# Kernel optimization log

Hardware: AMD Instinct MI355X
Metric: run time of the kernel (lower is better)

## Reference

```python
import jax, jax.numpy as jnp
import numpy as np

M = N = 768
Q = 32
P_ROW = P_COL = 4
NB_ITER = 3


def cheb_basis(L, order):
    # Chebyshev polynomials T_k(L), stacked -> (order+1, n, n)
    n = L.shape[0]
    Ts = [jnp.eye(n, dtype=L.dtype)]
    if order > 0:
        Ts.append(L)
    for _ in range(2, order + 1):
        Ts.append(2.0 * (L @ Ts[-1]) - Ts[-2])
    return jnp.stack(Ts)


def setup_inputs() -> dict:
    key = jax.random.key(0)
    ks = jax.random.split(key, 24)
    f32 = jnp.float32
    # scaled symmetric Laplacians with small spectral radius (keeps Cheb recursion stable)
    Ar = jax.random.normal(ks[0], (M, M), dtype=f32)
    L_row = (Ar + Ar.T) / (2.0 * jnp.sqrt(jnp.float32(M)))
    Ac = jax.random.normal(ks[1], (N, N), dtype=f32)
    L_col = (Ac + Ac.T) / (2.0 * jnp.sqrt(jnp.float32(N)))
    x = jax.random.normal(ks[2], (M, N), dtype=f32)
    theta = 0.05 * jax.random.normal(ks[3], (P_ROW + 1, P_COL + 1, Q), dtype=f32)
    bias = jnp.zeros((Q,), dtype=f32)
    s = 1.0 / np.sqrt(Q)
    def w(k):
        return s * jax.random.normal(k, (Q, Q), dtype=f32)
    inp = {
        'x': x, 'L_row': L_row, 'L_col': L_col, 'theta': theta, 'bias': bias,
        'W_f': w(ks[4]), 'U_f': w(ks[5]), 'b_f': jnp.zeros((Q,), f32),
        'W_i': w(ks[6]), 'U_i': w(ks[7]), 'b_i': jnp.zeros((Q,), f32),
        'W_o': w(ks[8]), 'U_o': w(ks[9]), 'b_o': jnp.zeros((Q,), f32),
        'W_c': w(ks[10]), 'U_c': w(ks[11]), 'b_c': jnp.zeros((Q,), f32),
        'W_out': s * jax.random.normal(ks[12], (Q, 1), dtype=f32),
        'b_out': jnp.zeros((1, 1), f32),
        'nb_iterations_rnn': NB_ITER,
    }
    return inp


def reference(x, L_row, L_col, theta, bias,
              W_f, U_f, b_f, W_i, U_i, b_i, W_o, U_o, b_o, W_c, U_c, b_c,
              W_out, b_out, nb_iterations_rnn):
    pr = theta.shape[0] - 1
    pc = theta.shape[1] - 1
    q = theta.shape[2]
    m, n = x.shape
    Tr = cheb_basis(L_row, pr)  # (pr+1, M, M)
    Tc = cheb_basis(L_col, pc)  # (pc+1, N, N)

    def conv(xx):
        xr = jnp.einsum('imp,pn->imn', Tr, xx)            # (pr+1, M, N)
        bf = jnp.einsum('imn,jnk->ijmk', xr, Tc)           # (pr+1, pc+1, M, N)
        return jnp.einsum('ijmn,ijo->omn', bf, theta) + bias[:, None, None]

    def step(carry, _):
        xx, h, c = carry
        xc = conv(xx).transpose(1, 2, 0).reshape(-1, q)    # (M*N, q)
        f = jax.nn.sigmoid(xc @ W_f + h @ U_f + b_f)
        i = jax.nn.sigmoid(xc @ W_i + h @ U_i + b_i)
        o = jax.nn.sigmoid(xc @ W_o + h @ U_o + b_o)
        cu = jax.nn.sigmoid(xc @ W_c + h @ U_c + b_c)      # note: sigmoid, as in source
        c = f * c + i * cu
        h = o * jax.nn.sigmoid(c)                           # note: sigmoid(c), as in source
        dx = jnp.tanh(c @ W_out + b_out).reshape(m, n)
        return (xx + dx, h, c), None

    h0 = jnp.zeros((m * n, q), dtype=x.dtype)
    c0 = jnp.zeros((m * n, q), dtype=x.dtype)
    (x_out, _, _), _ = jax.lax.scan(step, (x, h0, c0), None, length=int(nb_iterations_rnn))
    return x_out
```

## Files before the change

### kernel.cpp

```cpp
#include <hip/hip_runtime.h>
#include <hip/hip_bf16.h>
#include <stdint.h>


#define DIM 768
#define MXK 589824
#define STK 2949120

typedef _Float16 f16x8 __attribute__((ext_vector_type(8)));
typedef float f32x4 __attribute__((ext_vector_type(4)));
typedef unsigned short ushort_t;
typedef _Float16 f16_t;

__device__ __forceinline__ float sigm(float v) {
    float e = __expf(-v);
    return __builtin_amdgcn_rcpf(1.0f + e);
}
__device__ __forceinline__ void split2h(float f, f16_t& h1, f16_t& h2) {
    h1 = (f16_t)f;
    h2 = (f16_t)(f - (float)h1);
}

__device__ __forceinline__ void gl_lds16(const f16_t* g, f16_t* l) {
    auto gp = reinterpret_cast<const __attribute__((address_space(1))) uint32_t*>(
        reinterpret_cast<uintptr_t>(g));
    auto lp = reinterpret_cast<__attribute__((address_space(3))) uint32_t*>(
        reinterpret_cast<uintptr_t>(l));
    __builtin_amdgcn_global_load_lds(gp, lp, 16, 0, 0);
}

__global__ __launch_bounds__(256) void init_split(
    const float* __restrict__ Lrow, const float* __restrict__ Lcol,
    f16_t* __restrict__ S0, f16_t* __restrict__ S1)
{
    int idx = blockIdx.x * 256 + threadIdx.x;
    int p = idx / DIM, m = idx % DIM;
    f16_t eye = (p == m) ? (f16_t)1.0f : (f16_t)0.0f;
    S0[idx] = eye; S1[idx] = (f16_t)0.0f;
    S0[STK + idx] = eye; S1[STK + idx] = (f16_t)0.0f;
    f16_t h1, h2;
    split2h(Lrow[idx], h1, h2);
    S0[MXK + idx] = h1; S1[MXK + idx] = h2;
    split2h(Lcol[idx], h1, h2);
    S0[STK + MXK + idx] = h1; S1[STK + MXK + idx] = h2;
}

__global__ __launch_bounds__(256) void prep_gate(
    const float* __restrict__ Wf, const float* __restrict__ Wi,
    const float* __restrict__ Wo, const float* __restrict__ Wc,
    const float* __restrict__ Uf, const float* __restrict__ Ui,
    const float* __restrict__ Uo, const float* __restrict__ Uc,
    const float* __restrict__ theta, const float* __restrict__ biasv,
    f16_t* __restrict__ Wstack, f16_t* __restrict__ thstack)
{
    int idx = blockIdx.x * 256 + threadIdx.x;
    if (idx < 8192) {
        int R = idx >> 6, k = idx & 63;
        int g = (R >> 4) & 3, o = (R >> 6) * 16 + (R & 15);
        const float* Wg[4] = {Wf, Wi, Wo, Wc};
        const float* Ug[4] = {Uf, Ui, Uo, Uc};
        float v = (k < 32) ? Wg[g][k * 32 + o] : Ug[g][(k - 32) * 32 + o];
        Wstack[idx] = (f16_t)v;
    } else if (idx < 9216) {
        int t = idx - 8192;
        int o = t >> 5, k = t & 31;
        float v = (k < 25) ? theta[k * 32 + o]
                           : (k == 25 ? biasv[o] : 0.0f);
        thstack[o * 32 + k] = (f16_t)v;
    }
}

__global__ __launch_bounds__(256) void transpose_cvt2x(
    const float* __restrict__ in, f16_t* __restrict__ o1,
    f16_t* __restrict__ o2, f16_t* __restrict__ xr0,
    f16_t* __restrict__ Cbf)
{
    __shared__ float t[32][33];
    int x = threadIdx.x & 31, y = threadIdx.x >> 5;
    int bx = blockIdx.x * 32, by = blockIdx.y * 32;
#pragma unroll
    for (int r = 0; r < 4; ++r) {
        int p = by + y + 8 * r, q = bx + x;
        size_t oi = (size_t)p * DIM + q;
        float v = in[oi];
        t[y + 8 * r][x] = v;
        f16_t hv = (f16_t)v;
        xr0[oi] = hv;
        Cbf[(size_t)p * 3840 + q] = hv;
    }
    __syncthreads();
#pragma unroll
    for (int r = 0; r < 4; ++r) {
        float v = t[x][y + 8 * r];
        f16_t h1, h2;
        split2h(v, h1, h2);
        size_t o = (size_t)(bx + y + 8 * r) * DIM + by + x;
        o1[o] = h1; o2[o] = h2;
    }
}

__global__ __launch_bounds__(256, 4) void gemm_bt_h2(
    const f16_t* __restrict__ A1,
    const f16_t* __restrict__ B1, const f16_t* __restrict__ B2,
    const f16_t* __restrict__ P1, const f16_t* __restrict__ P2,
    f16_t* __restrict__ D1, f16_t* __restrict__ D2, f16_t* __restrict__ D3,
    int K, int ldc, int mode, int nbx, int halfStride, int coloff)
{
    __shared__ __align__(16) f16_t sA[2][128 * 32];
    __shared__ __align__(16) f16_t sB[2][2 * 96 * 32];

    const int tid = threadIdx.x;
    const bool dual = (B2 != nullptr);

    int bx, by;
    size_t hoff = 0;
    int aoff = 0, boff = 0, poff = 0, doff = 0;
    if (mode == 3) {
        int g = blockIdx.x;
        int sup = g >> 8;
        int rows0 = sup * 8;
        int H = 30 - rows0; if (H > 8) H = 8;
        int local = g - rows0 * nbx;
        by = rows0 + local % H;
        bx = local / H;
    } else if (mode == 4) {
        int g = blockIdx.x;
        int t34 = g / 96, r = g % 96;
        int stack = r / 48, rr = r % 48;
        by = rr >> 3; bx = rr & 7;
        hoff = (size_t)stack * halfStride;
        if (t34 == 0) { aoff = MXK; boff = 2 * MXK; poff = MXK; doff = 3 * MXK; }
        else          { aoff = 2 * MXK; boff = 2 * MXK; poff = 0; doff = 4 * MXK; }
    } else {
        bx = blockIdx.x % nbx;
        by = blockIdx.x / nbx;
        if (mode == 2 && by >= 6) { by -= 6; hoff = (size_t)halfStride; }
    }
    const int m0 = by * 128, n0 = bx * 96;

    const f16_t* Asrc1 = A1 + hoff + aoff;
    const f16_t* Bsrc1 = B1 + hoff + boff;
    const f16_t* Bsrc2 = dual ? B2 + hoff + boff : nullptr;
    const f16_t* Pq1 = P1 ? P1 + hoff + poff : nullptr;
    const f16_t* Pq2 = P2 ? P2 + hoff + poff : nullptr;
    f16_t* Dq1 = D1 + hoff + doff;
    f16_t* Dq2 = D2 ? D2 + hoff + doff : nullptr;

    const int lane = tid & 63, w4 = tid >> 6;
    const int wm = (w4 & 1) * 64, wn = (w4 >> 1) * 48;
    const int lm = lane & 15, quad = lane >> 4;
    const int psw = (quad ^ ((lm >> 1) & 3)) * 8;

    const f16_t* gApt[2]; int aslot[2];
#pragma unroll
    for (int cc = 0; cc < 2; ++cc) {
        int s = cc * 256 + w4 * 64 + lane;
        int row = s >> 2, pos = s & 3;
        int chunk = pos ^ ((row >> 1) & 3);
        gApt[cc] = Asrc1 + (size_t)(m0 + row) * K + chunk * 8;
        aslot[cc] = s * 8;
    }
    const f16_t* gBpt[3]; int bslot[3]; bool bact[3];
#pragma unroll
    for (int cc = 0; cc < 3; ++cc) {
        int slot = cc * 256 + w4 * 64 + lane;
        bact[cc] = dual || (slot < 384);
        int lev = slot >= 384 ? 1 : 0;
        int s = slot - lev * 384;
        int row = s >> 2, pos = s & 3;
        int chunk = pos ^ ((row >> 1) & 3);
        const f16_t* bs = (lev && dual) ? Bsrc2 : Bsrc1;
        gBpt[cc] = bs + (size_t)(n0 + row) * K + chunk * 8;
        bslot[cc] = lev * 3072 + s * 8;
    }

    f32x4 acc[4][3] = {};

#pragma unroll
    for (int cc = 0; cc < 2; ++cc) gl_lds16(gApt[cc], &sA[0][aslot[cc]]);
#pragma unroll
    for (int cc = 0; cc < 3; ++cc)
        if (bact[cc]) gl_lds16(gBpt[cc], &sB[0][bslot[cc]]);
    __syncthreads();

    int ib = 0;
    for (int kb = 0; kb < K; kb += 32, ib ^= 1) {
        if (kb + 32 < K) {
            int nb = ib ^ 1;
#pragma unroll
            for (int cc = 0; cc < 2; ++cc)
                gl_lds16(gApt[cc] + kb + 32, &sA[nb][aslot[cc]]);
#pragma unroll
            for (int cc = 0; cc < 3; ++cc)
                if (bact[cc]) gl_lds16(gBpt[cc] + kb + 32, &sB[nb][bslot[cc]]);
        }

        f16x8 bfr[2][3];
#pragma unroll
        for (int fn = 0; fn < 3; ++fn)
            bfr[0][fn] = *(const f16x8*)&sB[ib][(wn + fn * 16 + lm) * 32 + psw];
        if (dual) {
#pragma unroll
            for (int fn = 0; fn < 3; ++fn)
                bfr[1][fn] = *(const f16x8*)&sB[ib][3072 +
                                                (wn + fn * 16 + lm) * 32 + psw];
        }
#pragma unroll
        for (int fm = 0; fm < 4; ++fm) {
            f16x8 a1v = *(const f16x8*)&sA[ib][(wm + fm * 16 + lm) * 32 + psw];
#pragma unroll
            for (int fn = 0; fn < 3; ++fn) {
                acc[fm][fn] = __builtin_amdgcn_mfma_f32_16x16x32_f16(
                    a1v, bfr[0][fn], acc[fm][fn], 0, 0, 0);
                if (dual)
                    acc[fm][fn] = __builtin_amdgcn_mfma_f32_16x16x32_f16(
                        a1v, bfr[1][fn], acc[fm][fn], 0, 0, 0);
            }
        }
        __syncthreads();
    }

#pragma unroll
    for (int fm = 0; fm < 4; ++fm)
#pragma unroll
        for (int fn = 0; fn < 3; ++fn) {
            int col = n0 + wn + fn * 16 + lm;
#pragma unroll
            for (int r = 0; r < 4; ++r) {
                int row = m0 + wm + fm * 16 + quad * 4 + r;
                float val = acc[fm][fn][r];
                if (mode == 3) {
                    Dq1[(size_t)row * ldc + coloff + col] = (f16_t)val;
                } else if (mode == 1) {
                    Dq1[(size_t)row * ldc + col] = (f16_t)val;
                    if (D3) D3[(size_t)row * 3840 + col] = (f16_t)val;
                } else {
                    size_t o = (size_t)row * ldc + col;
                    val = 2.0f * val - ((float)Pq1[o] + (float)Pq2[o]);
                    f16_t h1, h2;
                    split2h(val, h1, h2);
                    Dq1[o] = h1; Dq2[o] = h2;
                }
            }
        }
}

__global__ __launch_bounds__(256, 3) void gate_theta_mfma(
    const f16_t* __restrict__ Cbf, const f16_t* __restrict__ thstack,
    const f16_t* __restrict__ Wstack,
    const float* __restrict__ bfv, const float* __restrict__ biv,
    const float* __restrict__ bov, const float* __restrict__ bcv,
    const float* __restrict__ Wout, const float* __restrict__ bout,
    f16_t* __restrict__ h, f16_t* __restrict__ c, float* __restrict__ x,
    int first, int last)
{
    __shared__ __align__(16) ushort_t sC[2][26 * 128];
    __shared__ __align__(16) ushort_t sB[2][128 * 40];
    __shared__ float red[256];

    const int tid = threadIdx.x;
    const int lane = tid & 63, w4 = tid >> 6;
    const int wm = (w4 & 1) * 64, wn = (w4 >> 1) * 64;
    const int lm = lane & 15, quad = lane >> 4;
    const int m = blockIdx.x;
    const int o0 = (wm >> 2) + quad * 4;
    const int pw = w4 * 32;

    if (tid < 32) {
        uint4 ones;
        ones.x = ones.y = ones.z = ones.w = 0x3C003C00u;
        *(uint4*)&sC[tid >> 4][25 * 128 + (tid & 15) * 8] = ones;
    }

    auto stage = [&](int n0, int buf) {
#pragma unroll
        for (int cc = 0; cc < 2; ++cc) {
            int s = cc * 256 + tid;
            if (s < 400) {
                int ij = s >> 4, f = s & 15;
                int i5 = (ij * 205) >> 10;
                int j5 = ij - i5 * 5;
                size_t ga = (size_t)(i5 * DIM + m) * 3840 + j5 * DIM + n0 + f * 8;
                gl_lds16(&Cbf[ga], (f16_t*)&sC[buf][ij * 128 + f * 8]);
            }
        }
    };

    f16x8 bth[2];
#pragma unroll
    for (int fn = 0; fn < 2; ++fn)
        bth[fn] = *(const f16x8*)&thstack[(fn * 16 + lm) * 32 + quad * 8];
    f16x8 af[4][2];
#pragma unroll
    for (int fm = 0; fm < 4; ++fm)
#pragma unroll
        for (int kc = 0; kc < 2; ++kc)
            af[fm][kc] = *(const f16x8*)&Wstack[(wm + fm * 16 + lm) * 64 +
                                                kc * 32 + quad * 8];
    const float4 bgf = *(const float4*)&bfv[o0];
    const float4 bgi = *(const float4*)&biv[o0];
    const float4 bgo = *(const float4*)&bov[o0];
    const float4 bgc = *(const float4*)&bcv[o0];
    const float4 wo4 = *(const float4*)&Wout[o0];
    float bf4[4] = {bgf.x, bgf.y, bgf.z, bgf.w};
    float bi4[4] = {bgi.x, bgi.y, bgi.z, bgi.w};
    float bo4[4] = {bgo.x, bgo.y, bgo.z, bgo.w};
    float bc4[4] = {bgc.x, bgc.y, bgc.z, bgc.w};
    float wo[4] = {wo4.x, wo4.y, wo4.z, wo4.w};
    const float bout0 = bout[0];

    stage(0, 0);
    f16x8 hfr[4];
    f16_t cold[4][4];
    if (!first) {
#pragma unroll
        for (int fn = 0; fn < 4; ++fn) {
            size_t p = (size_t)(m * DIM + wn + fn * 16 + lm);
            hfr[fn] = *(const f16x8*)&h[p * 32 + quad * 8];
            *(uint2*)cold[fn] = *(const uint2*)&c[p * 32 + o0];
        }
    } else {
#pragma unroll
        for (int fn = 0; fn < 4; ++fn) {
#pragma unroll
            for (int j = 0; j < 8; ++j) hfr[fn][j] = (f16_t)0.0f;
#pragma unroll
            for (int r = 0; r < 4; ++r) cold[fn][r] = (f16_t)0.0f;
        }
    }
    __syncthreads();

    int tb = 0;
    for (int t = 0; t < 6; ++t, tb ^= 1) {
        const int n0 = t * 128;
        const int pbase = m * DIM + n0;

        {
            const f16_t* sCf = (const f16_t*)sC[tb];
            f32x4 tacc[2][2] = {};
            f16x8 a0, a1;
#pragma unroll
            for (int j = 0; j < 8; ++j) {
                int k = quad * 8 + j;
                int ij = k > 25 ? 25 : k;
                a0[j] = sCf[ij * 128 + pw + lm];
                a1[j] = sCf[ij * 128 + pw + 16 + lm];
            }
#pragma unroll
            for (int fn = 0; fn < 2; ++fn) {
                tacc[0][fn] = __builtin_amdgcn_mfma_f32_16x16x32_f16(
                    a0, bth[fn], tacc[0][fn], 0, 0, 0);
                tacc[1][fn] = __builtin_amdgcn_mfma_f32_16x16x32_f16(
                    a1, bth[fn], tacc[1][fn], 0, 0, 0);
            }
#pragma unroll
            for (int fm2 = 0; fm2 < 2; ++fm2)
#pragma unroll
                for (int fn = 0; fn < 2; ++fn)
#pragma unroll
                    for (int r = 0; r < 4; ++r) {
                        f16_t hv = (f16_t)tacc[fm2][fn][r];
                        sB[tb][(pw + fm2 * 16 + quad * 4 + r) * 40 +
                               fn * 16 + lm] = __builtin_bit_cast(ushort_t, hv);
                    }
        }
        __syncthreads();

        if (t < 5) stage(n0 + 128, tb ^ 1);
        f16x8 hfrn[4];
        f16_t coldn[4][4];
        if (t < 5 && !first) {
#pragma unroll
            for (int fn = 0; fn < 4; ++fn) {
                size_t p = (size_t)(pbase + 128 + wn + fn * 16 + lm);
                hfrn[fn] = *(const f16x8*)&h[p * 32 + quad * 8];
                *(uint2*)coldn[fn] = *(const uint2*)&c[p * 32 + o0];
            }
        } else {
#pragma unroll
            for (int fn = 0; fn < 4; ++fn) {
#pragma unroll
                for (int j = 0; j < 8; ++j) hfrn[fn][j] = (f16_t)0.0f;
#pragma unroll
                for (int r = 0; r < 4; ++r) coldn[fn][r] = (f16_t)0.0f;
            }
        }

#pragma unroll
        for (int fn = 0; fn < 4; ++fn) {
            f16x8 bxc = *(const f16x8*)&sB[tb][(wn + fn * 16 + lm) * 40 +
                                              quad * 8];
            f32x4 acc[4] = {};
#pragma unroll
            for (int fm = 0; fm < 4; ++fm) {
                acc[fm] = __builtin_amdgcn_mfma_f32_16x16x32_f16(
                    af[fm][0], bxc, acc[fm], 0, 0, 0);
                acc[fm] = __builtin_amdgcn_mfma_f32_16x16x32_f16(
                    af[fm][1], hfr[fn], acc[fm], 0, 0, 0);
            }

            int px = wn + fn * 16 + lm;
            size_t p = (size_t)(pbase + px);
            f16_t cn16[4], hn16[4];
            float part = 0.f;
#pragma unroll
            for (int r = 0; r < 4; ++r) {
                float fg = sigm(acc[0][r] + bf4[r]);
                float ig = sigm(acc[1][r] + bi4[r]);
                float og = sigm(acc[2][r] + bo4[r]);
                float gg = sigm(acc[3][r] + bc4[r]);
                float cn = fg * (float)cold[fn][r] + ig * gg;
                cn16[r] = (f16_t)cn;
                hn16[r] = (f16_t)(og * sigm(cn));
                part = fmaf(cn, wo[r], part);
            }
            if (!last) {
                *(uint2*)&c[p * 32 + o0] = *(const uint2*)cn16;
                *(uint2*)&h[p * 32 + o0] = *(const uint2*)hn16;
            }
            part += __shfl_xor(part, 16, 64);
            part += __shfl_xor(part, 32, 64);
            if (quad == 0) red[px * 2 + (wm >> 6)] = part;
        }
        __syncthreads();

        if (tid < 128) {
            float v = red[tid * 2] + red[tid * 2 + 1] + bout0;
            v = fminf(fmaxf(v, -15.f), 15.f);
            float e = __expf(2.f * v);
            x[pbase + tid] += (e - 1.f) * __builtin_amdgcn_rcpf(e + 1.f);
        }

#pragma unroll
        for (int fn = 0; fn < 4; ++fn) {
            hfr[fn] = hfrn[fn];
#pragma unroll
            for (int r = 0; r < 4; ++r) cold[fn][r] = coldn[fn][r];
        }
    }
}

extern "C" void kernel_launch(void* const* d_in, const int* in_sizes, int n_in,
                              void* d_out, int out_size, void* d_ws, size_t ws_size,
                              hipStream_t stream)
{
    const float* x_in  = (const float*)d_in[0];
    const float* Lrow  = (const float*)d_in[1];
    const float* Lcol  = (const float*)d_in[2];
    const float* theta = (const float*)d_in[3];
    const float* bias  = (const float*)d_in[4];
    const float* Wf = (const float*)d_in[5];
    const float* Uf = (const float*)d_in[6];
    const float* bf = (const float*)d_in[7];
    const float* Wi = (const float*)d_in[8];
    const float* Ui = (const float*)d_in[9];
    const float* bi = (const float*)d_in[10];
    const float* Wo = (const float*)d_in[11];
    const float* Uo = (const float*)d_in[12];
    const float* bo = (const float*)d_in[13];
    const float* Wc = (const float*)d_in[14];
    const float* Uc = (const float*)d_in[15];
    const float* bc = (const float*)d_in[16];
    const float* Wout = (const float*)d_in[17];
    const float* bout = (const float*)d_in[18];
    (void)in_sizes; (void)n_in; (void)out_size;

    float* out = (float*)d_out;

    f16_t* base = (f16_t*)d_ws;
    f16_t* Cbf  = base;
    f16_t* h    = Cbf + 14745600;
    f16_t* c    = h + 18874368;
    f16_t* S0   = c + 18874368;
    f16_t* S1   = S0 + 2 * STK;
    f16_t* XR0  = S1 + 2 * STK;
    f16_t* Wstack  = XR0 + STK;
    f16_t* thstack = Wstack + 8192;
    f16_t* xT0  = thstack + 1024;
    f16_t* xT1  = xT0 + MXK;
    if (ws_size < (size_t)136857600) return;

    hipMemcpyAsync(out, x_in, (size_t)MXK * 4, hipMemcpyDeviceToDevice, stream);

    prep_gate<<<36, 256, 0, stream>>>(Wf, Wi, Wo, Wc, Uf, Ui, Uo, Uc, theta,
                                      bias, Wstack, thstack);
    init_split<<<MXK / 256, 256, 0, stream>>>(Lrow, Lcol, S0, S1);
    gemm_bt_h2<<<96, 256, 0, stream>>>(
        S0 + MXK, S0 + MXK, S1 + MXK, S0, S1,
        S0 + 2 * MXK, S1 + 2 * MXK, nullptr,
        DIM, DIM, 2, 8, STK, 0);
    gemm_bt_h2<<<192, 256, 0, stream>>>(
        S0, S0, S1, S0, S1, S0, S1, nullptr,
        DIM, DIM, 4, 8, STK, 0);

    for (int it = 0; it < 3; ++it) {
        transpose_cvt2x<<<dim3(24, 24), 256, 0, stream>>>(out, xT0, xT1,
                                                          XR0, Cbf);
        gemm_bt_h2<<<192, 256, 0, stream>>>(
            S0 + MXK, xT0, xT1,
            nullptr, nullptr,
            XR0 + MXK, nullptr, Cbf + (size_t)DIM * 3840,
            DIM, DIM, 1, 8, 0, 0);
        gemm_bt_h2<<<960, 256, 0, stream>>>(
            XR0, S0 + STK + MXK, nullptr,
            nullptr, nullptr,
            Cbf, nullptr, nullptr, DIM, 3840, 3, 32, 0, DIM);
        gate_theta_mfma<<<768, 256, 0, stream>>>(
            Cbf, thstack, Wstack,
            bf, bi, bo, bc, Wout, bout, h, c, out,
            it == 0 ? 1 : 0, it == 2 ? 1 : 0);
    }
}
```

Baseline: 442.5 us.

## Software-pipeline gate kernel: prefetch two tiles ahead and defer tanh tail

Restructures the per-tile loop of the fused gate kernel so staging runs two tiles ahead, the theta MFMA for the next tile is computed before the current tile's gate math, and the x-update tail is deferred to the next iteration using a double-buffered reduction array. This removes one __syncthreads per tile and lets global loads, theta contraction and gate math overlap. In exchange the loop carries more live state, which may raise register pressure under the 3-blocks launch bound, and buffer reuse across stage/theta/gate must stay race-free.

```diff
diff --git a/kernel.cpp b/kernel.cpp
--- a/kernel.cpp
+++ b/kernel.cpp
@@ -256,7 +256,7 @@
 {
     __shared__ __align__(16) ushort_t sC[2][26 * 128];
     __shared__ __align__(16) ushort_t sB[2][128 * 40];
-    __shared__ float red[256];
+    __shared__ float red[2][256];
 
     const int tid = threadIdx.x;
     const int lane = tid & 63, w4 = tid >> 6;
@@ -309,7 +309,48 @@
     float wo[4] = {wo4.x, wo4.y, wo4.z, wo4.w};
     const float bout0 = bout[0];
 
+    auto theta = [&](int sbuf, int dbuf) {
+        const f16_t* sCf = (const f16_t*)sC[sbuf];
+        f32x4 tacc[2][2] = {};
+        f16x8 a0, a1;
+#pragma unroll
+        for (int j = 0; j < 8; ++j) {
+            int k = quad * 8 + j;
+            int ij = k > 25 ? 25 : k;
+            a0[j] = sCf[ij * 128 + pw + lm];
+            a1[j] = sCf[ij * 128 + pw + 16 + lm];
+        }
+#pragma unroll
+        for (int fn = 0; fn < 2; ++fn) {
+            tacc[0][fn] = __builtin_amdgcn_mfma_f32_16x16x32_f16(
+                a0, bth[fn], tacc[0][fn], 0, 0, 0);
+            tacc[1][fn] = __builtin_amdgcn_mfma_f32_16x16x32_f16(
+                a1, bth[fn], tacc[1][fn], 0, 0, 0);
+        }
+#pragma unroll
+        for (int fm2 = 0; fm2 < 2; ++fm2)
+#pragma unroll
+            for (int fn = 0; fn < 2; ++fn)
+#pragma unroll
+                for (int r = 0; r < 4; ++r) {
+                    f16_t hv = (f16_t)tacc[fm2][fn][r];
+                    sB[dbuf][(pw + fm2 * 16 + quad * 4 + r) * 40 +
+                             fn * 16 + lm] = __builtin_bit_cast(ushort_t, hv);
+                }
+    };
+
+    auto tail = [&](int t) {
+        if (tid < 128) {
+            float v = red[t & 1][tid * 2] + red[t & 1][tid * 2 + 1] + bout0;
+            v = fminf(fmaxf(v, -15.f), 15.f);
+            float e = __expf(2.f * v);
+            x[m * DIM + t * 128 + tid] +=
+                (e - 1.f) * __builtin_amdgcn_rcpf(e + 1.f);
+        }
+    };
+
     stage(0, 0);
+    stage(128, 1);
     f16x8 hfr[4];
     f16_t cold[4][4];
     if (!first) {
@@ -329,60 +370,35 @@
         }
     }
     __syncthreads();
-
-    int tb = 0;
-    for (int t = 0; t < 6; ++t, tb ^= 1) {
-        const int n0 = t * 128;
-        const int pbase = m * DIM + n0;
-
-        {
-            const f16_t* sCf = (const f16_t*)sC[tb];
-            f32x4 tacc[2][2] = {};
-            f16x8 a0, a1;
-#pragma unroll
-            for (int j = 0; j < 8; ++j) {
-                int k = quad * 8 + j;
-                int ij = k > 25 ? 25 : k;
-                a0[j] = sCf[ij * 128 + pw + lm];
-                a1[j] = sCf[ij * 128 + pw + 16 + lm];
-            }
-#pragma unroll
-            for (int fn = 0; fn < 2; ++fn) {
-                tacc[0][fn] = __builtin_amdgcn_mfma_f32_16x16x32_f16(
-                    a0, bth[fn], tacc[0][fn], 0, 0, 0);
-                tacc[1][fn] = __builtin_amdgcn_mfma_f32_16x16x32_f16(
-                    a1, bth[fn], tacc[1][fn], 0, 0, 0);
-            }
-#pragma unroll
-            for (int fm2 = 0; fm2 < 2; ++fm2)
-#pragma unroll
-                for (int fn = 0; fn < 2; ++fn)
-#pragma unroll
-                    for (int r = 0; r < 4; ++r) {
-                        f16_t hv = (f16_t)tacc[fm2][fn][r];
-                        sB[tb][(pw + fm2 * 16 + quad * 4 + r) * 40 +
-                               fn * 16 + lm] = __builtin_bit_cast(ushort_t, hv);
-                    }
-        }
-        __syncthreads();
-
-        if (t < 5) stage(n0 + 128, tb ^ 1);
-        f16x8 hfrn[4];
-        f16_t coldn[4][4];
-        if (t < 5 && !first) {
+    theta(0, 0);
+    __syncthreads();
+
+    for (int t = 0; t < 6; ++t) {
+        const int tb = t & 1;
+        const int pbase = m * DIM + t * 128;
+
+        if (t > 0) tail(t - 1);
+
+        if (t + 2 < 6) stage((t + 2) * 128, tb);
+
+        if (t + 1 < 6) theta(tb ^ 1, tb ^ 1);
+
+        f16x8 hfr2[4];
+        f16_t cold2[4][4];
+        if (t + 1 < 6 && !first) {
 #pragma unroll
             for (int fn = 0; fn < 4; ++fn) {
                 size_t p = (size_t)(pbase + 128 + wn + fn * 16 + lm);
-                hfrn[fn] = *(const f16x8*)&h[p * 32 + quad * 8];
-                *(uint2*)coldn[fn] = *(const uint2*)&c[p * 32 + o0];
+                hfr2[fn] = *(const f16x8*)&h[p * 32 + quad * 8];
+                *(uint2*)cold2[fn] = *(const uint2*)&c[p * 32 + o0];
             }
         } else {
 #pragma unroll
             for (int fn = 0; fn < 4; ++fn) {
 #pragma unroll
-                for (int j = 0; j < 8; ++j) hfrn[fn][j] = (f16_t)0.0f;
-#pragma unroll
-                for (int r = 0; r < 4; ++r) coldn[fn][r] = (f16_t)0.0f;
+                for (int j = 0; j < 8; ++j) hfr2[fn][j] = (f16_t)0.0f;
+#pragma unroll
+                for (int r = 0; r < 4; ++r) cold2[fn][r] = (f16_t)0.0f;
             }
         }
 
@@ -420,24 +436,19 @@
             }
             part += __shfl_xor(part, 16, 64);
             part += __shfl_xor(part, 32, 64);
-            if (quad == 0) red[px * 2 + (wm >> 6)] = part;
-        }
+            if (quad == 0) red[tb][px * 2 + (wm >> 6)] = part;
+        }
+
         __syncthreads();
 
-        if (tid < 128) {
-            float v = red[tid * 2] + red[tid * 2 + 1] + bout0;
-            v = fminf(fmaxf(v, -15.f), 15.f);
-            float e = __expf(2.f * v);
-            x[pbase + tid] += (e - 1.f) * __builtin_amdgcn_rcpf(e + 1.f);
-        }
-
 #pragma unroll
         for (int fn = 0; fn < 4; ++fn) {
-            hfr[fn] = hfrn[fn];
-#pragma unroll
-            for (int r = 0; r < 4; ++r) cold[fn][r] = coldn[fn][r];
-        }
-    }
+            hfr[fn] = hfr2[fn];
+#pragma unroll
+            for (int r = 0; r < 4; ++r) cold[fn][r] = cold2[fn][r];
+        }
+    }
+    tail(5);
 }
 
 extern "C" void kernel_launch(void* const* d_in, const int* in_sizes, int n_in,
```

Result: no change. 438.8 us (-0.8%).

## Split gate kernel rows across two blocks and raise occupancy

Applied to the files above, without the earlier changes.

Each gate block now handles half of a matrix row, 384 columns over 3 tiles, so the grid doubles to 1536 blocks. Launch bounds rise from 3 to 5 blocks per CU. To make room, the staged-product LDS buffer is single-buffered and the register prefetch of the next tile's h/c state is dropped. The intent is more resident waves to hide memory latency in the gate/LSTM stage, at the cost of exposing h/c load latency within each tile and repeating per-block setup such as weight fragment loads.

```diff
diff --git a/kernel.cpp b/kernel.cpp
--- a/kernel.cpp
+++ b/kernel.cpp
@@ -245,7 +245,7 @@
         }
 }
 
-__global__ __launch_bounds__(256, 3) void gate_theta_mfma(
+__global__ __launch_bounds__(256, 5) void gate_theta_mfma(
     const f16_t* __restrict__ Cbf, const f16_t* __restrict__ thstack,
     const f16_t* __restrict__ Wstack,
     const float* __restrict__ bfv, const float* __restrict__ biv,
@@ -255,14 +255,15 @@
     int first, int last)
 {
     __shared__ __align__(16) ushort_t sC[2][26 * 128];
-    __shared__ __align__(16) ushort_t sB[2][128 * 40];
+    __shared__ __align__(16) ushort_t sB[128 * 40];
     __shared__ float red[256];
 
     const int tid = threadIdx.x;
     const int lane = tid & 63, w4 = tid >> 6;
     const int wm = (w4 & 1) * 64, wn = (w4 >> 1) * 64;
     const int lm = lane & 15, quad = lane >> 4;
-    const int m = blockIdx.x;
+    const int m = blockIdx.x >> 1;
+    const int colbase = (blockIdx.x & 1) * 384;
     const int o0 = (wm >> 2) + quad * 4;
     const int pw = w4 * 32;
 
@@ -272,7 +273,8 @@
         *(uint4*)&sC[tid >> 4][25 * 128 + (tid & 15) * 8] = ones;
     }
 
-    auto stage = [&](int n0, int buf) {
+    auto stage = [&](int t, int buf) {
+        int n0 = colbase + t * 128;
 #pragma unroll
         for (int cc = 0; cc < 2; ++cc) {
             int s = cc * 256 + tid;
@@ -310,30 +312,12 @@
     const float bout0 = bout[0];
 
     stage(0, 0);
-    f16x8 hfr[4];
-    f16_t cold[4][4];
-    if (!first) {
-#pragma unroll
-        for (int fn = 0; fn < 4; ++fn) {
-            size_t p = (size_t)(m * DIM + wn + fn * 16 + lm);
-            hfr[fn] = *(const f16x8*)&h[p * 32 + quad * 8];
-            *(uint2*)cold[fn] = *(const uint2*)&c[p * 32 + o0];
-        }
-    } else {
-#pragma unroll
-        for (int fn = 0; fn < 4; ++fn) {
-#pragma unroll
-            for (int j = 0; j < 8; ++j) hfr[fn][j] = (f16_t)0.0f;
-#pragma unroll
-            for (int r = 0; r < 4; ++r) cold[fn][r] = (f16_t)0.0f;
-        }
-    }
+    stage(1, 1);
     __syncthreads();
 
-    int tb = 0;
-    for (int t = 0; t < 6; ++t, tb ^= 1) {
-        const int n0 = t * 128;
-        const int pbase = m * DIM + n0;
+    for (int t = 0; t < 3; ++t) {
+        const int tb = t & 1;
+        const int pbase = m * DIM + colbase + t * 128;
 
         {
             const f16_t* sCf = (const f16_t*)sC[tb];
@@ -360,36 +344,37 @@
 #pragma unroll
                     for (int r = 0; r < 4; ++r) {
                         f16_t hv = (f16_t)tacc[fm2][fn][r];
-                        sB[tb][(pw + fm2 * 16 + quad * 4 + r) * 40 +
-                               fn * 16 + lm] = __builtin_bit_cast(ushort_t, hv);
+                        sB[(pw + fm2 * 16 + quad * 4 + r) * 40 +
+                           fn * 16 + lm] = __builtin_bit_cast(ushort_t, hv);
                     }
         }
         __syncthreads();
 
-        if (t < 5) stage(n0 + 128, tb ^ 1);
-        f16x8 hfrn[4];
-        f16_t coldn[4][4];
-        if (t < 5 && !first) {
+        if (t == 0) stage(2, 0);
+
+        f16x8 hfr[4];
+        f16_t cold[4][4];
+        if (!first) {
 #pragma unroll
             for (int fn = 0; fn < 4; ++fn) {
-                size_t p = (size_t)(pbase + 128 + wn + fn * 16 + lm);
-                hfrn[fn] = *(const f16x8*)&h[p * 32 + quad * 8];
-                *(uint2*)coldn[fn] = *(const uint2*)&c[p * 32 + o0];
+                size_t p = (size_t)(pbase + wn + fn * 16 + lm);
+                hfr[fn] = *(const f16x8*)&h[p * 32 + quad * 8];
+                *(uint2*)cold[fn] = *(const uint2*)&c[p * 32 + o0];
             }
         } else {
 #pragma unroll
             for (int fn = 0; fn < 4; ++fn) {
 #pragma unroll
-                for (int j = 0; j < 8; ++j) hfrn[fn][j] = (f16_t)0.0f;
-#pragma unroll
-                for (int r = 0; r < 4; ++r) coldn[fn][r] = (f16_t)0.0f;
+                for (int j = 0; j < 8; ++j) hfr[fn][j] = (f16_t)0.0f;
+#pragma unroll
+                for (int r = 0; r < 4; ++r) cold[fn][r] = (f16_t)0.0f;
             }
         }
 
 #pragma unroll
         for (int fn = 0; fn < 4; ++fn) {
-            f16x8 bxc = *(const f16x8*)&sB[tb][(wn + fn * 16 + lm) * 40 +
-                                              quad * 8];
+            f16x8 bxc = *(const f16x8*)&sB[(wn + fn * 16 + lm) * 40 +
+                                           quad * 8];
             f32x4 acc[4] = {};
 #pragma unroll
             for (int fm = 0; fm < 4; ++fm) {
@@ -429,13 +414,6 @@
             v = fminf(fmaxf(v, -15.f), 15.f);
             float e = __expf(2.f * v);
             x[pbase + tid] += (e - 1.f) * __builtin_amdgcn_rcpf(e + 1.f);
-        }
-
-#pragma unroll
-        for (int fn = 0; fn < 4; ++fn) {
-            hfr[fn] = hfrn[fn];
-#pragma unroll
-            for (int r = 0; r < 4; ++r) cold[fn][r] = coldn[fn][r];
         }
     }
 }
@@ -505,7 +483,7 @@
             XR0, S0 + STK + MXK, nullptr,
             nullptr, nullptr,
             Cbf, nullptr, nullptr, DIM, 3840, 3, 32, 0, DIM);
-        gate_theta_mfma<<<768, 256, 0, stream>>>(
+        gate_theta_mfma<<<1536, 256, 0, stream>>>(
             Cbf, thstack, Wstack,
             bf, bi, bo, bc, Wout, bout, h, c, out,
             it == 0 ? 1 : 0, it == 2 ? 1 : 0);
```

Result: slower. 587.1 us (+32.7%).
